# Performance work log

Hardware: AMD Instinct MI355X
Metric: run time of the kernel (lower is better)

## Reference

```python
import jax, jax.numpy as jnp
import numpy as np

B, D, K, NUM_CLASSES = 8192, 512, 20, 1024
EPS = 1e-12  # torch F.normalize clamp


def setup_inputs() -> dict:
    key = jax.random.key(0)
    k1, k2 = jax.random.split(key)
    batch = jax.random.normal(k1, (B, D), dtype=jnp.float32)
    labels = jax.random.randint(k2, (B,), 0, NUM_CLASSES, dtype=jnp.int64 if jax.config.jax_enable_x64 else jnp.int32)
    return {"batch": batch, "labels": labels, "k": K}


def reference(batch, labels, k):
    # L2-normalize rows (F.normalize, p=2)
    norm = jnp.maximum(jnp.linalg.norm(batch, axis=1, keepdims=True), EPS)
    x = batch / norm
    cos = x @ x.T                                   # [B, B] cosine similarity
    min_value = cos.min() - 1.0                     # scalar, computed before diag fill
    bs = cos.shape[0]
    diag = jnp.eye(bs, dtype=bool)
    cos = jnp.where(diag, min_value, cos)           # fill_diagonal_(min_value)
    # argsort(-cos)[:, :k]  ==  top-k by similarity (self excluded via diag fill)
    top_vals, top_idx = jax.lax.top_k(cos, k)       # [B, k]
    # preds = (cos + 1)/2 gathered at neighbor indices == (top_vals + 1)/2
    preds = (top_vals + 1.0) * 0.5
    true_labels = (labels[top_idx] == labels[:, None]).astype(jnp.float32)  # [B, k]
    # nn.BCELoss with mean reduction; torch clamps each log term at -100
    logp = jnp.maximum(jnp.log(preds), -100.0)
    log1mp = jnp.maximum(jnp.log1p(-preds), -100.0)
    loss = -(true_labels * logp + (1.0 - true_labels) * log1mp)
    return loss.mean()
```

## Files before the change

### kernel.cpp

```cpp
#include <hip/hip_runtime.h>
#include <hip/hip_bf16.h>

#define NROWS 8192
#define DIM   512
#define KSEL  20
#define NSURV 384
#define NTRI  2080

typedef unsigned int u32;
typedef unsigned long long u64;
typedef short bf16x8 __attribute__((ext_vector_type(8)));
typedef float f32x4 __attribute__((ext_vector_type(4)));
typedef ushort u16x2 __attribute__((ext_vector_type(2)));

typedef const void __attribute__((address_space(1))) as1_void;
typedef void __attribute__((address_space(3))) as3_void;

__device__ __forceinline__ void async_ld16(const ushort* g, ushort* l) {
    __builtin_amdgcn_global_load_lds((as1_void*)g, (as3_void*)l, 16, 0, 0);
}

__device__ __forceinline__ ushort f2bf(float f) {
    u32 u = __float_as_uint(f);
    return (ushort)((u + 0x7FFFu + ((u >> 16) & 1u)) >> 16);
}

__device__ __forceinline__ u32 mono16(u32 r) {
    return r ^ (0x8000u | ((r >> 15) * 0x7FFFu));
}
__device__ __forceinline__ u32 mono2(u32 w) {
    return w ^ (0x80008000u | (((w >> 15) & 0x10001u) * 0x7FFFu));
}
__device__ __forceinline__ u32 mkey(float f) { return mono16((u32)f2bf(f)); }

__device__ __forceinline__ u32 pkmax(u32 a, u32 b) {
    union { u32 u; u16x2 v; } x, y; x.u = a; y.u = b;
    x.v = __builtin_elementwise_max(x.v, y.v);
    return x.u;
}
__device__ __forceinline__ u32 pkmin(u32 a, u32 b) {
    union { u32 u; u16x2 v; } x, y; x.u = a; y.u = b;
    x.v = __builtin_elementwise_min(x.v, y.v);
    return x.u;
}

__device__ __forceinline__ void tri_idx(int t, int& by, int& bx) {
    by = (int)((sqrtf(8.0f * (float)t + 1.0f) - 1.0f) * 0.5f);
    while ((by + 1) * (by + 2) / 2 <= t) ++by;
    while (by * (by + 1) / 2 > t) --by;
    bx = t - by * (by + 1) / 2;
}

__device__ __forceinline__ void append(u32* lists, u32* cnts, int row, u32 val) {
    u32 o = atomicAdd(&cnts[row], 1u);
    if (o < NSURV) lists[(size_t)row * NSURV + o] = val;
}

__global__ __launch_bounds__(256) void k_norm(const float* __restrict__ x,
                                              ushort* __restrict__ xn) {
    int lane = threadIdx.x & 63;
    int wv   = threadIdx.x >> 6;
    int row  = blockIdx.x * 4 + wv;
    const float4* xr = (const float4*)(x + (size_t)row * DIM);
    float4 a = xr[2 * lane];
    float4 b = xr[2 * lane + 1];
    float ss = a.x*a.x + a.y*a.y + a.z*a.z + a.w*a.w
             + b.x*b.x + b.y*b.y + b.z*b.z + b.w*b.w;
    #pragma unroll
    for (int off = 32; off; off >>= 1) ss += __shfl_xor(ss, off);
    float sc = 1.0f / fmaxf(sqrtf(ss), 1e-12f);
    float v[8] = {a.x*sc, a.y*sc, a.z*sc, a.w*sc, b.x*sc, b.y*sc, b.z*sc, b.w*sc};
    union { ushort u[8]; uint4 q; } o;
    #pragma unroll
    for (int i = 0; i < 8; ++i) o.u[i] = f2bf(v[i]);
    *(uint4*)(xn + (size_t)row * DIM + lane * 8) = o.q;
}

__global__ __launch_bounds__(256) void k_gemm(const ushort* __restrict__ xn,
                                              ushort* __restrict__ C,
                                              ushort* __restrict__ M) {
    __shared__ ushort sh[2 * 128 * 64];
    ushort* lA = sh;
    ushort* lB = sh + 128 * 64;
    int tid  = threadIdx.x;
    int lane = tid & 63, wv = tid >> 6;
    int wr = wv >> 1, wc = wv & 1;
    int q = lane >> 4, m = lane & 15;
    int bx, by;
    tri_idx(blockIdx.x, by, bx);
    int grow0 = by * 128;
    int gcol0 = bx * 128;
    f32x4 acc[4][4] = {};

    int lr = lane >> 3;
    int lc = lane & 7;
    for (int kc = 0; kc < 8; ++kc) {
        #pragma unroll
        for (int t = 0; t < 4; ++t) {
            int rb  = wv * 32 + t * 8;
            int r   = rb + lr;
            int fch = lc ^ (r & 7);
            async_ld16(xn + (size_t)(grow0 + r) * DIM + kc * 64 + fch * 8, &lA[rb * 64]);
            async_ld16(xn + (size_t)(gcol0 + r) * DIM + kc * 64 + fch * 8, &lB[rb * 64]);
        }
        __syncthreads();
        #pragma unroll
        for (int s = 0; s < 2; ++s) {
            bf16x8 af[4], bfr[4];
            #pragma unroll
            for (int i = 0; i < 4; ++i) {
                int ra = wr * 64 + i * 16 + m;
                af[i]  = *(const bf16x8*)&lA[ra * 64 + (((s * 4 + q) ^ (ra & 7)) * 8)];
                int rb2 = wc * 64 + i * 16 + m;
                bfr[i] = *(const bf16x8*)&lB[rb2 * 64 + (((s * 4 + q) ^ (rb2 & 7)) * 8)];
            }
            #pragma unroll
            for (int i = 0; i < 4; ++i)
                #pragma unroll
                for (int j = 0; j < 4; ++j)
                    acc[i][j] = __builtin_amdgcn_mfma_f32_16x16x32_bf16(af[i], bfr[j], acc[i][j], 0, 0, 0);
        }
        __syncthreads();
    }

    size_t tb = (size_t)blockIdx.x * 16384;
    float cmf[4] = {-3.0f, -3.0f, -3.0f, -3.0f};
    #pragma unroll
    for (int i = 0; i < 4; ++i) {
        float rmf[4] = {-3.0f, -3.0f, -3.0f, -3.0f};
        int rloc = wr * 64 + i * 16 + q * 4;
        #pragma unroll
        for (int j = 0; j < 4; ++j) {
            int cl = wc * 64 + j * 16 + m;
            int c  = gcol0 + cl;
            ushort sv[4];
            #pragma unroll
            for (int reg = 0; reg < 4; ++reg) {
                int grw  = grow0 + rloc + reg;
                float a  = acc[i][j][reg];
                bool dg  = (grw == c);
                float mv = dg ? -3.0f : a;
                rmf[reg] = fmaxf(rmf[reg], mv);
                cmf[j]   = fmaxf(cmf[j], mv);
                sv[reg]  = dg ? (ushort)0xC040 : f2bf(a);
            }
            uint2 o = { (u32)sv[0] | ((u32)sv[1] << 16),
                        (u32)sv[2] | ((u32)sv[3] << 16) };
            *(uint2*)&C[tb + (size_t)(((wv * 16 + i * 4 + j) * 64) + lane) * 4] = o;
        }
        u32 p01 = mkey(rmf[0]) | (mkey(rmf[1]) << 16);
        u32 p23 = mkey(rmf[2]) | (mkey(rmf[3]) << 16);
        #pragma unroll
        for (int off = 1; off <= 8; off <<= 1) {
            p01 = pkmax(p01, (u32)__shfl_xor((int)p01, off));
            p23 = pkmax(p23, (u32)__shfl_xor((int)p23, off));
        }
        if (m == 0) {
            size_t mb = (size_t)(grow0 + rloc) * 128 + bx * 2 + wc;
            M[mb]       = (ushort)(p01 & 0xFFFFu);
            M[mb + 128] = (ushort)(p01 >> 16);
            M[mb + 256] = (ushort)(p23 & 0xFFFFu);
            M[mb + 384] = (ushort)(p23 >> 16);
        }
    }
    if (bx != by) {
        u32 q01 = mkey(cmf[0]) | (mkey(cmf[1]) << 16);
        u32 q23 = mkey(cmf[2]) | (mkey(cmf[3]) << 16);
        q01 = pkmax(q01, (u32)__shfl_xor((int)q01, 16));
        q01 = pkmax(q01, (u32)__shfl_xor((int)q01, 32));
        q23 = pkmax(q23, (u32)__shfl_xor((int)q23, 16));
        q23 = pkmax(q23, (u32)__shfl_xor((int)q23, 32));
        if (q == 0) {
            int gc = gcol0 + wc * 64 + m;
            int sg = by * 2 + wr;
            M[(size_t)(gc +  0) * 128 + sg] = (ushort)(q01 & 0xFFFFu);
            M[(size_t)(gc + 16) * 128 + sg] = (ushort)(q01 >> 16);
            M[(size_t)(gc + 32) * 128 + sg] = (ushort)(q23 & 0xFFFFu);
            M[(size_t)(gc + 48) * 128 + sg] = (ushort)(q23 >> 16);
        }
    }
}

__global__ __launch_bounds__(256) void k_thresh(const ushort* __restrict__ M,
                                                ushort* __restrict__ T) {
    int lane = threadIdx.x & 63;
    int wv   = threadIdx.x >> 6;
    int row  = blockIdx.x * 4 + wv;
    u32 pm  = *(const u32*)&M[(size_t)row * 128 + 2 * lane];
    u32 klo = pm & 0xFFFFu, khi = pm >> 16;
    u32 Tv = 0;
    #pragma unroll
    for (int b = 15; b >= 0; --b) {
        u32 cand = Tv | (1u << b);
        int c = __popcll(__ballot(klo >= cand)) + __popcll(__ballot(khi >= cand));
        if (c >= KSEL) Tv = cand;
    }
    if (Tv == 0) Tv = 1;
    if (lane == 0) T[row] = (ushort)Tv;
}

__global__ __launch_bounds__(256) void k_scan(const ushort* __restrict__ C,
                                              const ushort* __restrict__ T,
                                              u32* __restrict__ lists,
                                              u32* __restrict__ cnts) {
    int by, bx;
    tri_idx(blockIdx.x, by, bx);
    const ushort* tile = C + (size_t)blockIdx.x * 16384;
    int tid = threadIdx.x;
    bool diag = (bx == by);
    #pragma unroll
    for (int s = 0; s < 8; ++s) {
        int e0 = s * 2048 + tid * 8;
        uint4 v = *(const uint4*)&tile[e0];
        int sub   = e0 >> 8;
        int wv2   = sub >> 4, ii = (sub >> 2) & 3, jj = sub & 3;
        int lane0 = (e0 >> 2) & 63;
        int qq = lane0 >> 4, m0 = lane0 & 15;
        int gr0 = by * 128 + (wv2 >> 1) * 64 + ii * 16 + qq * 4;
        int gc0 = bx * 128 + (wv2 & 1) * 64 + jj * 16 + m0;
        uint2 trw = *(const uint2*)&T[gr0];
        u32   tc2 = *(const u32*)&T[gc0];
        u32 k0 = mono2(v.x), k1 = mono2(v.y), k2 = mono2(v.z), k3 = mono2(v.w);
        u32 pmx = pkmax(pkmax(k0, k1), pkmax(k2, k3));
        u32 mx  = max(pmx & 0xFFFFu, pmx >> 16);
        u32 rm2 = pkmin(trw.x, trw.y);
        u32 rmn = min(rm2 & 0xFFFFu, rm2 >> 16);
        u32 cmn = min(tc2 & 0xFFFFu, tc2 >> 16);
        u32 thr = diag ? rmn : min(rmn, cmn);
        if (mx < thr) continue;
        u32 ks[4]  = { k0, k1, k2, k3 };
        u32 trs[4] = { trw.x, trw.y, trw.x, trw.y };
        u32 tcs[4] = { tc2 & 0xFFFFu, tc2 & 0xFFFFu, tc2 >> 16, tc2 >> 16 };
        int cls[4] = { gc0, gc0, gc0 + 1, gc0 + 1 };
        int rws[4] = { gr0, gr0 + 2, gr0, gr0 + 2 };
        #pragma unroll
        for (int h = 0; h < 4; ++h) {
            u32 kA = ks[h] & 0xFFFFu, kB = ks[h] >> 16;
            u32 tA = trs[h] & 0xFFFFu, tB = trs[h] >> 16;
            int rA = rws[h], rB = rws[h] + 1, cc = cls[h];
            if (kA >= tA) append(lists, cnts, rA, (kA << 16) | (u32)cc);
            if (kB >= tB) append(lists, cnts, rB, (kB << 16) | (u32)cc);
            if (!diag) {
                u32 tc = tcs[h];
                if (kA >= tc) append(lists, cnts, cc, (kA << 16) | (u32)rA);
                if (kB >= tc) append(lists, cnts, cc, (kB << 16) | (u32)rB);
            }
        }
    }
}

__global__ __launch_bounds__(256) void k_topk(const u32* __restrict__ lists,
                                              const u32* __restrict__ cnts,
                                              const int* __restrict__ labels,
                                              float* __restrict__ partials) {
    int lane = threadIdx.x & 63;
    int wv   = threadIdx.x >> 6;
    int row  = blockIdx.x * 4 + wv;
    u32 cnt = min(cnts[row], (u32)NSURV);
    const u32* L = lists + (size_t)row * NSURV;
    int mylab = labels[row];
    float loss = 0.0f;

    if (cnt <= 64u) {
        u32 gg  = ((u32)lane < cnt) ? L[lane] : 0u;
        u32 key = gg >> 16;
        u32 V = 0;
        #pragma unroll
        for (int b = 15; b >= 0; --b) {
            u32 cand = V | (1u << b);
            if (__popcll(__ballot(key >= cand)) >= KSEL) V = cand;
        }
        int cgt  = __popcll(__ballot(key > V));
        int ceq  = __popcll(__ballot(gg != 0 && key == V));
        int need = KSEL - cgt;
        bool incl;
        if (ceq == need) {
            incl = (gg != 0) && (key >= V);
        } else {
            u32 col = gg & 0xFFFFu;
            bool tie = (gg != 0) && (key == V);
            u32 Cv = 0;
            #pragma unroll
            for (int b = 15; b >= 0; --b) {
                u32 cand2 = Cv | (1u << b);
                if (__popcll(__ballot(tie && col >= cand2)) >= need) Cv = cand2;
            }
            incl = (key > V) || (tie && col >= Cv);
        }
        if (incl) {
            u32 col = gg & 0xFFFFu;
            u32 raw = (key & 0x8000u) ? (key ^ 0x8000u) : (key ^ 0xFFFFu);
            float v = __uint_as_float(raw << 16);
            float p = (v + 1.0f) * 0.5f;
            bool tm = (labels[col] == mylab);
            loss -= tm ? fmaxf(logf(p), -100.0f) : fmaxf(log1pf(-p), -100.0f);
        }
    } else {
        u32 g[6];
        #pragma unroll
        for (int j = 0; j < 6; ++j) {
            u32 idx = (u32)lane + (u32)j * 64u;
            g[j] = (idx < cnt) ? L[idx] : 0u;
        }
        u32 V = 0;
        #pragma unroll
        for (int b = 15; b >= 0; --b) {
            u32 cand = V | (1u << b);
            int c = 0;
            #pragma unroll
            for (int j = 0; j < 6; ++j)
                c += __popcll(__ballot((g[j] >> 16) >= cand));
            if (c >= KSEL) V = cand;
        }
        int cgt = 0, ceq = 0;
        #pragma unroll
        for (int j = 0; j < 6; ++j) {
            cgt += __popcll(__ballot(g[j] != 0 && (g[j] >> 16) > V));
            ceq += __popcll(__ballot(g[j] != 0 && (g[j] >> 16) == V));
        }
        int need = KSEL - cgt;
        bool all_ties = (ceq == need);
        #pragma unroll
        for (int j = 0; j < 6; ++j) {
            u32 key = g[j] >> 16, col = g[j] & 0xFFFFu;
            if (g[j] != 0 && (key > V || (all_ties && key == V))) {
                u32 raw = (key & 0x8000u) ? (key ^ 0x8000u) : (key ^ 0xFFFFu);
                float v = __uint_as_float(raw << 16);
                float p = (v + 1.0f) * 0.5f;
                bool tm = (labels[col] == mylab);
                loss -= tm ? fmaxf(logf(p), -100.0f) : fmaxf(log1pf(-p), -100.0f);
            }
        }
        if (!all_ties) {
            for (int r = 0; r < need; ++r) {
                u32 best = 0;
                #pragma unroll
                for (int j = 0; j < 6; ++j) {
                    u32 c2 = (g[j] != 0 && (g[j] >> 16) == V) ? ((g[j] & 0xFFFFu) + 1u) : 0u;
                    best = max(best, c2);
                }
                #pragma unroll
                for (int off = 32; off; off >>= 1) best = max(best, (u32)__shfl_xor((int)best, off));
                #pragma unroll
                for (int j = 0; j < 6; ++j) {
                    if (g[j] != 0 && (g[j] >> 16) == V && ((g[j] & 0xFFFFu) + 1u) == best) {
                        u32 col = g[j] & 0xFFFFu;
                        u32 raw = (V & 0x8000u) ? (V ^ 0x8000u) : (V ^ 0xFFFFu);
                        float v = __uint_as_float(raw << 16);
                        float p = (v + 1.0f) * 0.5f;
                        bool tm = (labels[col] == mylab);
                        loss -= tm ? fmaxf(logf(p), -100.0f) : fmaxf(log1pf(-p), -100.0f);
                        g[j] = 0;
                    }
                }
            }
        }
    }

    #pragma unroll
    for (int off = 32; off; off >>= 1) loss += __shfl_xor(loss, off);
    if (lane == 0) partials[row] = loss;
}

__global__ __launch_bounds__(256) void k_final(const float* __restrict__ partials,
                                               float* __restrict__ out) {
    __shared__ float s[4];
    int tid = threadIdx.x, lane = tid & 63, wvi = tid >> 6;
    const float4* p4 = (const float4*)partials;
    float sum = 0.0f;
    #pragma unroll
    for (int i = 0; i < 8; ++i) {
        float4 v = p4[tid + i * 256];
        sum += v.x + v.y + v.z + v.w;
    }
    #pragma unroll
    for (int off = 32; off; off >>= 1) sum += __shfl_xor(sum, off);
    if (lane == 0) s[wvi] = sum;
    __syncthreads();
    if (tid == 0) out[0] = (s[0] + s[1] + s[2] + s[3]) * (1.0f / (float)(NROWS * KSEL));
}

extern "C" void kernel_launch(void* const* d_in, const int* in_sizes, int n_in,
                              void* d_out, int out_size, void* d_ws, size_t ws_size,
                              hipStream_t stream) {
    const float* batch  = (const float*)d_in[0];
    const int*   labels = (const int*)d_in[1];

    ushort* xn = (ushort*)d_ws;
    ushort* C  = xn + (size_t)NROWS * DIM;

    char* scr = (char*)d_in[0];
    ushort* M        = (ushort*)scr;
    ushort* T        = (ushort*)(scr + (2u << 20));
    u32*    cnts     = (u32*)  (scr + (2u << 20) + (64u << 10));
    float*  partials = (float*)(scr + (2u << 20) + (128u << 10));
    u32*    lists    = (u32*)  (scr + (4u << 20));

    k_norm<<<NROWS / 4, 256, 0, stream>>>(batch, xn);
    hipMemsetAsync(cnts, 0, NROWS * sizeof(u32), stream);
    k_gemm  <<<NTRI,      256, 0, stream>>>(xn, C, M);
    k_thresh<<<NROWS / 4, 256, 0, stream>>>(M, T);
    k_scan  <<<NTRI,      256, 0, stream>>>(C, T, lists, cnts);
    k_topk  <<<NROWS / 4, 256, 0, stream>>>(lists, cnts, labels, partials);
    k_final <<<1,         256, 0, stream>>>(partials, (float*)d_out);
}
```

Before: 177.5 us.

## Remap GEMM tiles per XCD, batch scan loads, fold final reduction into atomics

The GEMM's block index is remapped so each group of 260 consecutive triangle tiles lands on the same XCD under round-robin dispatch. The aim is better L2 reuse of the shared row and column panels. The scan kernel now issues all eight tile loads and threshold loads before processing them, to expose more memory-level parallelism. The per-row partials array and its full reduction kernel are replaced by a per-block atomicAdd into one accumulator, which the memset now also zeroes; this leaves a trivial final scale kernel and makes the float summation order nondeterministic.

```diff
diff --git a/kernel.cpp b/kernel.cpp
--- a/kernel.cpp
+++ b/kernel.cpp
@@ -86,8 +86,10 @@
     int lane = tid & 63, wv = tid >> 6;
     int wr = wv >> 1, wc = wv & 1;
     int q = lane >> 4, m = lane & 15;
+    int b0 = (int)blockIdx.x;
+    int tt = (b0 & 7) * 260 + (b0 >> 3);
     int bx, by;
-    tri_idx(blockIdx.x, by, bx);
+    tri_idx(tt, by, bx);
     int grow0 = by * 128;
     int gcol0 = bx * 128;
     f32x4 acc[4][4] = {};
@@ -123,7 +125,7 @@
         __syncthreads();
     }
 
-    size_t tb = (size_t)blockIdx.x * 16384;
+    size_t tb = (size_t)tt * 16384;
     float cmf[4] = {-3.0f, -3.0f, -3.0f, -3.0f};
     #pragma unroll
     for (int i = 0; i < 4; ++i) {
@@ -204,33 +206,49 @@
                                               u32* __restrict__ lists,
                                               u32* __restrict__ cnts) {
     int by, bx;
-    tri_idx(blockIdx.x, by, bx);
-    const ushort* tile = C + (size_t)blockIdx.x * 16384;
+    tri_idx((int)blockIdx.x, by, bx);
+    const uint4* tile4 = (const uint4*)(C + (size_t)blockIdx.x * 16384);
     int tid = threadIdx.x;
     bool diag = (bx == by);
+
+    uint4 v[8];
+    uint2 trw[8];
+    u32   tc2[8];
+    #pragma unroll
+    for (int s = 0; s < 8; ++s) v[s] = tile4[s * 256 + tid];
     #pragma unroll
     for (int s = 0; s < 8; ++s) {
-        int e0 = s * 2048 + tid * 8;
-        uint4 v = *(const uint4*)&tile[e0];
+        int e0    = (s * 256 + tid) * 8;
         int sub   = e0 >> 8;
         int wv2   = sub >> 4, ii = (sub >> 2) & 3, jj = sub & 3;
         int lane0 = (e0 >> 2) & 63;
         int qq = lane0 >> 4, m0 = lane0 & 15;
         int gr0 = by * 128 + (wv2 >> 1) * 64 + ii * 16 + qq * 4;
         int gc0 = bx * 128 + (wv2 & 1) * 64 + jj * 16 + m0;
-        uint2 trw = *(const uint2*)&T[gr0];
-        u32   tc2 = *(const u32*)&T[gc0];
-        u32 k0 = mono2(v.x), k1 = mono2(v.y), k2 = mono2(v.z), k3 = mono2(v.w);
+        trw[s] = *(const uint2*)&T[gr0];
+        tc2[s] = *(const u32*)&T[gc0];
+    }
+
+    #pragma unroll
+    for (int s = 0; s < 8; ++s) {
+        int e0    = (s * 256 + tid) * 8;
+        int sub   = e0 >> 8;
+        int wv2   = sub >> 4, ii = (sub >> 2) & 3, jj = sub & 3;
+        int lane0 = (e0 >> 2) & 63;
+        int qq = lane0 >> 4, m0 = lane0 & 15;
+        int gr0 = by * 128 + (wv2 >> 1) * 64 + ii * 16 + qq * 4;
+        int gc0 = bx * 128 + (wv2 & 1) * 64 + jj * 16 + m0;
+        u32 k0 = mono2(v[s].x), k1 = mono2(v[s].y), k2 = mono2(v[s].z), k3 = mono2(v[s].w);
         u32 pmx = pkmax(pkmax(k0, k1), pkmax(k2, k3));
         u32 mx  = max(pmx & 0xFFFFu, pmx >> 16);
-        u32 rm2 = pkmin(trw.x, trw.y);
+        u32 rm2 = pkmin(trw[s].x, trw[s].y);
         u32 rmn = min(rm2 & 0xFFFFu, rm2 >> 16);
-        u32 cmn = min(tc2 & 0xFFFFu, tc2 >> 16);
+        u32 cmn = min(tc2[s] & 0xFFFFu, tc2[s] >> 16);
         u32 thr = diag ? rmn : min(rmn, cmn);
         if (mx < thr) continue;
         u32 ks[4]  = { k0, k1, k2, k3 };
-        u32 trs[4] = { trw.x, trw.y, trw.x, trw.y };
-        u32 tcs[4] = { tc2 & 0xFFFFu, tc2 & 0xFFFFu, tc2 >> 16, tc2 >> 16 };
+        u32 trs[4] = { trw[s].x, trw[s].y, trw[s].x, trw[s].y };
+        u32 tcs[4] = { tc2[s] & 0xFFFFu, tc2[s] & 0xFFFFu, tc2[s] >> 16, tc2[s] >> 16 };
         int cls[4] = { gc0, gc0, gc0 + 1, gc0 + 1 };
         int rws[4] = { gr0, gr0 + 2, gr0, gr0 + 2 };
         #pragma unroll
@@ -252,7 +270,8 @@
 __global__ __launch_bounds__(256) void k_topk(const u32* __restrict__ lists,
                                               const u32* __restrict__ cnts,
                                               const int* __restrict__ labels,
-                                              float* __restrict__ partials) {
+                                              float* __restrict__ acc) {
+    __shared__ float sl[4];
     int lane = threadIdx.x & 63;
     int wv   = threadIdx.x >> 6;
     int row  = blockIdx.x * 4 + wv;
@@ -359,25 +378,13 @@
 
     #pragma unroll
     for (int off = 32; off; off >>= 1) loss += __shfl_xor(loss, off);
-    if (lane == 0) partials[row] = loss;
-}
-
-__global__ __launch_bounds__(256) void k_final(const float* __restrict__ partials,
-                                               float* __restrict__ out) {
-    __shared__ float s[4];
-    int tid = threadIdx.x, lane = tid & 63, wvi = tid >> 6;
-    const float4* p4 = (const float4*)partials;
-    float sum = 0.0f;
-    #pragma unroll
-    for (int i = 0; i < 8; ++i) {
-        float4 v = p4[tid + i * 256];
-        sum += v.x + v.y + v.z + v.w;
-    }
-    #pragma unroll
-    for (int off = 32; off; off >>= 1) sum += __shfl_xor(sum, off);
-    if (lane == 0) s[wvi] = sum;
+    if (lane == 0) sl[wv] = loss;
     __syncthreads();
-    if (tid == 0) out[0] = (s[0] + s[1] + s[2] + s[3]) * (1.0f / (float)(NROWS * KSEL));
+    if (threadIdx.x == 0) atomicAdd(acc, sl[0] + sl[1] + sl[2] + sl[3]);
+}
+
+__global__ void k_final(const float* __restrict__ acc, float* __restrict__ out) {
+    if (threadIdx.x == 0) out[0] = acc[0] * (1.0f / (float)(NROWS * KSEL));
 }
 
 extern "C" void kernel_launch(void* const* d_in, const int* in_sizes, int n_in,
@@ -390,17 +397,17 @@
     ushort* C  = xn + (size_t)NROWS * DIM;
 
     char* scr = (char*)d_in[0];
-    ushort* M        = (ushort*)scr;
-    ushort* T        = (ushort*)(scr + (2u << 20));
-    u32*    cnts     = (u32*)  (scr + (2u << 20) + (64u << 10));
-    float*  partials = (float*)(scr + (2u << 20) + (128u << 10));
-    u32*    lists    = (u32*)  (scr + (4u << 20));
+    ushort* M     = (ushort*)scr;
+    ushort* T     = (ushort*)(scr + (2u << 20));
+    u32*    cnts  = (u32*)  (scr + (2u << 20) + (64u << 10));
+    float*  acc   = (float*)(scr + (2u << 20) + (96u << 10));
+    u32*    lists = (u32*)  (scr + (3u << 20));
 
     k_norm<<<NROWS / 4, 256, 0, stream>>>(batch, xn);
-    hipMemsetAsync(cnts, 0, NROWS * sizeof(u32), stream);
+    hipMemsetAsync(cnts, 0, NROWS * sizeof(u32) + 256, stream);
     k_gemm  <<<NTRI,      256, 0, stream>>>(xn, C, M);
     k_thresh<<<NROWS / 4, 256, 0, stream>>>(M, T);
     k_scan  <<<NTRI,      256, 0, stream>>>(C, T, lists, cnts);
-    k_topk  <<<NROWS / 4, 256, 0, stream>>>(lists, cnts, labels, partials);
-    k_final <<<1,         256, 0, stream>>>(partials, (float*)d_out);
-}
+    k_topk  <<<NROWS / 4, 256, 0, stream>>>(lists, cnts, labels, acc);
+    k_final <<<1, 64, 0, stream>>>(acc, (float*)d_out);
+}
```

After: 203.0 us. +14.4%, slower.

## Recompute GEMM in filter pass instead of storing bf16 similarity matrix

Applied to the files above, without the earlier changes.

Stops writing the full bf16 similarity tiles to global memory and rereading them in the scan pass. A second GEMM pass recomputes each tile and filters candidates against the per-row thresholds straight from registers. Thresholds are staged in shared memory, and the triangular tile order is permuted so that consecutive blocks are spread across the 8-way split. This trades about 68 MB of global write and read traffic for doubling the MFMA work.

```diff
diff --git a/kernel.cpp b/kernel.cpp
--- a/kernel.cpp
+++ b/kernel.cpp
@@ -27,9 +27,6 @@
 
 __device__ __forceinline__ u32 mono16(u32 r) {
     return r ^ (0x8000u | ((r >> 15) * 0x7FFFu));
-}
-__device__ __forceinline__ u32 mono2(u32 w) {
-    return w ^ (0x80008000u | (((w >> 15) & 0x10001u) * 0x7FFFu));
 }
 __device__ __forceinline__ u32 mkey(float f) { return mono16((u32)f2bf(f)); }
 
@@ -76,22 +73,13 @@
     *(uint4*)(xn + (size_t)row * DIM + lane * 8) = o.q;
 }
 
-__global__ __launch_bounds__(256) void k_gemm(const ushort* __restrict__ xn,
-                                              ushort* __restrict__ C,
-                                              ushort* __restrict__ M) {
-    __shared__ ushort sh[2 * 128 * 64];
+__device__ __forceinline__ void gemm_kloop(const ushort* __restrict__ xn,
+                                           ushort* sh, int grow0, int gcol0,
+                                           int lane, int wv, f32x4 (&acc)[4][4]) {
     ushort* lA = sh;
     ushort* lB = sh + 128 * 64;
-    int tid  = threadIdx.x;
-    int lane = tid & 63, wv = tid >> 6;
     int wr = wv >> 1, wc = wv & 1;
     int q = lane >> 4, m = lane & 15;
-    int bx, by;
-    tri_idx(blockIdx.x, by, bx);
-    int grow0 = by * 128;
-    int gcol0 = bx * 128;
-    f32x4 acc[4][4] = {};
-
     int lr = lane >> 3;
     int lc = lane & 7;
     for (int kc = 0; kc < 8; ++kc) {
@@ -122,8 +110,23 @@
         }
         __syncthreads();
     }
-
-    size_t tb = (size_t)blockIdx.x * 16384;
+}
+
+__global__ __launch_bounds__(256) void k_gemm_digest(const ushort* __restrict__ xn,
+                                                     ushort* __restrict__ M) {
+    __shared__ ushort sh[2 * 128 * 64];
+    int tid  = threadIdx.x;
+    int lane = tid & 63, wv = tid >> 6;
+    int wr = wv >> 1, wc = wv & 1;
+    int q = lane >> 4, m = lane & 15;
+    int b0 = (int)blockIdx.x;
+    int tt = (b0 & 7) * 260 + (b0 >> 3);
+    int bx, by;
+    tri_idx(tt, by, bx);
+    int grow0 = by * 128, gcol0 = bx * 128;
+    f32x4 acc[4][4] = {};
+    gemm_kloop(xn, sh, grow0, gcol0, lane, wv, acc);
+
     float cmf[4] = {-3.0f, -3.0f, -3.0f, -3.0f};
     #pragma unroll
     for (int i = 0; i < 4; ++i) {
@@ -131,22 +134,15 @@
         int rloc = wr * 64 + i * 16 + q * 4;
         #pragma unroll
         for (int j = 0; j < 4; ++j) {
-            int cl = wc * 64 + j * 16 + m;
-            int c  = gcol0 + cl;
-            ushort sv[4];
+            int c = gcol0 + wc * 64 + j * 16 + m;
             #pragma unroll
             for (int reg = 0; reg < 4; ++reg) {
                 int grw  = grow0 + rloc + reg;
                 float a  = acc[i][j][reg];
-                bool dg  = (grw == c);
-                float mv = dg ? -3.0f : a;
+                float mv = (grw == c) ? -3.0f : a;
                 rmf[reg] = fmaxf(rmf[reg], mv);
                 cmf[j]   = fmaxf(cmf[j], mv);
-                sv[reg]  = dg ? (ushort)0xC040 : f2bf(a);
-            }
-            uint2 o = { (u32)sv[0] | ((u32)sv[1] << 16),
-                        (u32)sv[2] | ((u32)sv[3] << 16) };
-            *(uint2*)&C[tb + (size_t)(((wv * 16 + i * 4 + j) * 64) + lane) * 4] = o;
+            }
         }
         u32 p01 = mkey(rmf[0]) | (mkey(rmf[1]) << 16);
         u32 p23 = mkey(rmf[2]) | (mkey(rmf[3]) << 16);
@@ -199,51 +195,55 @@
     if (lane == 0) T[row] = (ushort)Tv;
 }
 
-__global__ __launch_bounds__(256) void k_scan(const ushort* __restrict__ C,
-                                              const ushort* __restrict__ T,
-                                              u32* __restrict__ lists,
-                                              u32* __restrict__ cnts) {
-    int by, bx;
-    tri_idx(blockIdx.x, by, bx);
-    const ushort* tile = C + (size_t)blockIdx.x * 16384;
-    int tid = threadIdx.x;
+__global__ __launch_bounds__(256) void k_gemm_filter(const ushort* __restrict__ xn,
+                                                     const ushort* __restrict__ T,
+                                                     u32* __restrict__ lists,
+                                                     u32* __restrict__ cnts) {
+    __shared__ ushort sh[2 * 128 * 64];
+    __shared__ ushort sTr[128];
+    __shared__ ushort sTc[128];
+    int tid  = threadIdx.x;
+    int lane = tid & 63, wv = tid >> 6;
+    int wr = wv >> 1, wc = wv & 1;
+    int q = lane >> 4, m = lane & 15;
+    int b0 = (int)blockIdx.x;
+    int tt = (b0 & 7) * 260 + (b0 >> 3);
+    int bx, by;
+    tri_idx(tt, by, bx);
+    int grow0 = by * 128, gcol0 = bx * 128;
     bool diag = (bx == by);
-    #pragma unroll
-    for (int s = 0; s < 8; ++s) {
-        int e0 = s * 2048 + tid * 8;
-        uint4 v = *(const uint4*)&tile[e0];
-        int sub   = e0 >> 8;
-        int wv2   = sub >> 4, ii = (sub >> 2) & 3, jj = sub & 3;
-        int lane0 = (e0 >> 2) & 63;
-        int qq = lane0 >> 4, m0 = lane0 & 15;
-        int gr0 = by * 128 + (wv2 >> 1) * 64 + ii * 16 + qq * 4;
-        int gc0 = bx * 128 + (wv2 & 1) * 64 + jj * 16 + m0;
-        uint2 trw = *(const uint2*)&T[gr0];
-        u32   tc2 = *(const u32*)&T[gc0];
-        u32 k0 = mono2(v.x), k1 = mono2(v.y), k2 = mono2(v.z), k3 = mono2(v.w);
-        u32 pmx = pkmax(pkmax(k0, k1), pkmax(k2, k3));
-        u32 mx  = max(pmx & 0xFFFFu, pmx >> 16);
+    if (tid < 64)       ((u32*)sTr)[tid]      = *(const u32*)&T[grow0 + tid * 2];
+    else if (tid < 128) ((u32*)sTc)[tid - 64] = *(const u32*)&T[gcol0 + (tid - 64) * 2];
+    f32x4 acc[4][4] = {};
+    gemm_kloop(xn, sh, grow0, gcol0, lane, wv, acc);
+
+    #pragma unroll
+    for (int i = 0; i < 4; ++i) {
+        int rloc = wr * 64 + i * 16 + q * 4;
+        uint2 trw = *(const uint2*)&sTr[rloc];
         u32 rm2 = pkmin(trw.x, trw.y);
         u32 rmn = min(rm2 & 0xFFFFu, rm2 >> 16);
-        u32 cmn = min(tc2 & 0xFFFFu, tc2 >> 16);
-        u32 thr = diag ? rmn : min(rmn, cmn);
-        if (mx < thr) continue;
-        u32 ks[4]  = { k0, k1, k2, k3 };
-        u32 trs[4] = { trw.x, trw.y, trw.x, trw.y };
-        u32 tcs[4] = { tc2 & 0xFFFFu, tc2 & 0xFFFFu, tc2 >> 16, tc2 >> 16 };
-        int cls[4] = { gc0, gc0, gc0 + 1, gc0 + 1 };
-        int rws[4] = { gr0, gr0 + 2, gr0, gr0 + 2 };
-        #pragma unroll
-        for (int h = 0; h < 4; ++h) {
-            u32 kA = ks[h] & 0xFFFFu, kB = ks[h] >> 16;
-            u32 tA = trs[h] & 0xFFFFu, tB = trs[h] >> 16;
-            int rA = rws[h], rB = rws[h] + 1, cc = cls[h];
-            if (kA >= tA) append(lists, cnts, rA, (kA << 16) | (u32)cc);
-            if (kB >= tB) append(lists, cnts, rB, (kB << 16) | (u32)cc);
-            if (!diag) {
-                u32 tc = tcs[h];
-                if (kA >= tc) append(lists, cnts, cc, (kA << 16) | (u32)rA);
-                if (kB >= tc) append(lists, cnts, cc, (kB << 16) | (u32)rB);
+        #pragma unroll
+        for (int j = 0; j < 4; ++j) {
+            int cl = wc * 64 + j * 16 + m;
+            int gc = gcol0 + cl;
+            u32 tc = (u32)sTc[cl];
+            u32 k[4];
+            #pragma unroll
+            for (int reg = 0; reg < 4; ++reg) {
+                int grw = grow0 + rloc + reg;
+                ushort sv = (grw == gc) ? (ushort)0xC040 : f2bf(acc[i][j][reg]);
+                k[reg] = mono16((u32)sv);
+            }
+            u32 kmax = max(max(k[0], k[1]), max(k[2], k[3]));
+            u32 thr  = diag ? rmn : min(rmn, tc);
+            if (kmax < thr) continue;
+            u32 tr4[4] = { trw.x & 0xFFFFu, trw.x >> 16, trw.y & 0xFFFFu, trw.y >> 16 };
+            #pragma unroll
+            for (int reg = 0; reg < 4; ++reg) {
+                int gr = grow0 + rloc + reg;
+                if (k[reg] >= tr4[reg]) append(lists, cnts, gr, (k[reg] << 16) | (u32)gc);
+                if (!diag && k[reg] >= tc) append(lists, cnts, gc, (k[reg] << 16) | (u32)gr);
             }
         }
     }
@@ -387,20 +387,19 @@
     const int*   labels = (const int*)d_in[1];
 
     ushort* xn = (ushort*)d_ws;
-    ushort* C  = xn + (size_t)NROWS * DIM;
 
     char* scr = (char*)d_in[0];
     ushort* M        = (ushort*)scr;
     ushort* T        = (ushort*)(scr + (2u << 20));
     u32*    cnts     = (u32*)  (scr + (2u << 20) + (64u << 10));
     float*  partials = (float*)(scr + (2u << 20) + (128u << 10));
-    u32*    lists    = (u32*)  (scr + (4u << 20));
+    u32*    lists    = (u32*)  (scr + (3u << 20));
 
     k_norm<<<NROWS / 4, 256, 0, stream>>>(batch, xn);
     hipMemsetAsync(cnts, 0, NROWS * sizeof(u32), stream);
-    k_gemm  <<<NTRI,      256, 0, stream>>>(xn, C, M);
-    k_thresh<<<NROWS / 4, 256, 0, stream>>>(M, T);
-    k_scan  <<<NTRI,      256, 0, stream>>>(C, T, lists, cnts);
-    k_topk  <<<NROWS / 4, 256, 0, stream>>>(lists, cnts, labels, partials);
-    k_final <<<1,         256, 0, stream>>>(partials, (float*)d_out);
-}
+    k_gemm_digest<<<NTRI,      256, 0, stream>>>(xn, M);
+    k_thresh     <<<NROWS / 4, 256, 0, stream>>>(M, T);
+    k_gemm_filter<<<NTRI,      256, 0, stream>>>(xn, T, lists, cnts);
+    k_topk       <<<NROWS / 4, 256, 0, stream>>>(lists, cnts, labels, partials);
+    k_final      <<<1,         256, 0, stream>>>(partials, (float*)d_out);
+}
```

Measured after the change: 221.1 us. +24.6%, slower.
